# Kernel tuning notes

Hardware: AMD Instinct MI355X
Metric: run time of the kernel (lower is better)

The kernel has to match this reference:

```python
import jax, jax.numpy as jnp
import numpy as np

B, F, N = 128, 256, 2000

def setup_inputs() -> dict:
    key = jax.random.key(0)
    ks = jax.random.split(key, 10)
    s = 0.05
    return {
        'nfeature': jax.random.normal(ks[0], (B, F, N, 1), jnp.float32),
        'last_current': jax.random.randint(ks[1], (B, 2), 0, N, jnp.int32),
        'Wg': jax.random.normal(ks[2], (F, F), jnp.float32) * s,
        'bg': jax.random.normal(ks[3], (F,), jnp.float32) * s,
        'Wnode': jax.random.normal(ks[4], (3 * F, F), jnp.float32) * s,
        'bnode': jax.random.normal(ks[5], (3 * F,), jnp.float32) * s,
        'Wlc': jax.random.normal(ks[6], (F, 2 * F), jnp.float32) * s,
        'blc': jax.random.normal(ks[7], (F,), jnp.float32) * s,
        'Wproj': jax.random.normal(ks[8], (F, F), jnp.float32) * s,
        'bproj': jax.random.normal(ks[9], (F,), jnp.float32) * s,
    }

def reference(nfeature, last_current, Wg, bg, Wnode, bnode, Wlc, blc, Wproj, bproj):
    # nfeature: [B, F, N, 1]
    x = nfeature[..., 0]                                  # [B, F, N]
    f = x.shape[1]
    scale = 1.0 / jnp.sqrt(jnp.asarray(f, x.dtype))
    # global fixed query: max over nodes then Linear
    glb = jnp.max(x, axis=2)                              # [B, F]
    Q = glb @ Wg.T + bg                                   # [B, F]
    # node embeddings via 1x1 conv == channel GEMM, split into K, V, logit_K
    kvl = jnp.einsum('bfn,gf->bgn', x, Wnode) + bnode[None, :, None]  # [B, 3F, N]
    K, V, Klog = jnp.split(kvl, 3, axis=1)                # each [B, F, N]
    # gather last/current city features
    lc = jnp.take_along_axis(x, last_current[:, None, :], axis=2)     # [B, F, 2]
    context = jnp.concatenate([lc[:, :, 0], lc[:, :, 1]], axis=1)     # [B, 2F]
    cQ = context @ Wlc.T + blc + Q                        # [B, F]
    # attention: single query over N keys
    ucj = jnp.einsum('bf,bfn->bn', cQ, K) * scale         # [B, N]
    attn = jax.nn.softmax(ucj, axis=1)
    nc = jnp.einsum('bn,bfn->bf', attn, V)                # [B, F]
    nc = nc @ Wproj.T + bproj                             # [B, F]
    logits = jnp.einsum('bf,bfn->bn', nc, Klog) * scale   # [B, N]
    return jnp.tanh(logits) * 10.0
```

## Files before the change

kernel.cpp:

```cpp
#include <hip/hip_runtime.h>
#include <hip/hip_fp16.h>
#include <math.h>

#define BB 128
#define FF 256
#define NN 2000
#define SW 8
#define SC 256

typedef float f32x4 __attribute__((ext_vector_type(4)));
union H8 { f32x4 v; __half2 h[4]; };

__device__ __forceinline__ float sel8(f32x4 a, f32x4 b, int e) {
    float v;
    switch (e) {
        case 0: v = a.x; break; case 1: v = a.y; break;
        case 2: v = a.z; break; case 3: v = a.w; break;
        case 4: v = b.x; break; case 5: v = b.y; break;
        case 6: v = b.z; break; default: v = b.w; break;
    }
    return v;
}

__device__ __forceinline__ float dot4(f32x4 a, f32x4 b) {
    float s = a.x * b.x;
    s = fmaf(a.y, b.y, s);
    s = fmaf(a.z, b.z, s);
    s = fmaf(a.w, b.w, s);
    return s;
}

__global__ __launch_bounds__(256) void k_convmax(const float* __restrict__ x,
                                                 const int* __restrict__ lc,
                                                 __half* __restrict__ xh,
                                                 float* __restrict__ glb,
                                                 float* __restrict__ xg) {
    int row  = (blockIdx.x << 2) | (threadIdx.x >> 6);
    int lane = threadIdx.x & 63;
    int b    = row >> 8;
    const int c0 = lc[2 * b], c1 = lc[2 * b + 1];
    const int i0 = c0 >> 3, e0 = c0 & 7;
    const int i1 = c1 >> 3, e1 = c1 & 7;
    const f32x4* src = (const f32x4*)(x + (size_t)row * NN);
    f32x4*       dst = (f32x4*)(xh + (size_t)row * NN);
    float m = -INFINITY;
    for (int i = lane; i < 250; i += 64) {
        f32x4 a = __builtin_nontemporal_load(src + 2 * i);
        f32x4 q = __builtin_nontemporal_load(src + 2 * i + 1);
        m = fmaxf(m, fmaxf(fmaxf(a.x, a.y), fmaxf(a.z, a.w)));
        m = fmaxf(m, fmaxf(fmaxf(q.x, q.y), fmaxf(q.z, q.w)));
        if (i == i0) xg[row * 2]     = sel8(a, q, e0);
        if (i == i1) xg[row * 2 + 1] = sel8(a, q, e1);
        H8 o;
        o.h[0] = __floats2half2_rn(a.x, a.y);
        o.h[1] = __floats2half2_rn(a.z, a.w);
        o.h[2] = __floats2half2_rn(q.x, q.y);
        o.h[3] = __floats2half2_rn(q.z, q.w);
        dst[i] = o.v;
    }
#pragma unroll
    for (int off = 32; off; off >>= 1) m = fmaxf(m, __shfl_xor(m, off));
    if (!lane) glb[row] = m;
}

__global__ __launch_bounds__(256) void k_prep(
    const float* __restrict__ xg, const float* __restrict__ glb,
    const float* __restrict__ Wg, const float* __restrict__ bg,
    const float* __restrict__ Wnode, const float* __restrict__ bnode,
    const float* __restrict__ Wlc, const float* __restrict__ blc,
    float* __restrict__ cK, float* __restrict__ cK0)
{
    int b = blockIdx.x, tid = threadIdx.x, w = tid >> 6, lane = tid & 63;
    __shared__ float s_glb[FF], s_ctx[2 * FF], s_cQ[FF], s_bias[FF], s_red[FF];
    s_glb[tid] = glb[b * FF + tid];
    float2 g2 = ((const float2*)xg)[b * FF + tid];
    s_ctx[tid]      = g2.x;
    s_ctx[FF + tid] = g2.y;
    s_bias[tid] = bg[tid] + blc[tid];
    __syncthreads();

    f32x4 gv  = *(const f32x4*)&s_glb[lane << 2];
    f32x4 c0v = *(const f32x4*)&s_ctx[lane << 3];
    f32x4 c1v = *(const f32x4*)&s_ctx[(lane << 3) + 4];

    for (int k = 0; k < 64; k += 4) {
        float p0, p1, p2, p3;
        {
            int fb = (w << 6) + k;
            f32x4 wg0 = *(const f32x4*)(Wg + (size_t)fb * FF + (lane << 2));
            f32x4 wg1 = *(const f32x4*)(Wg + (size_t)(fb + 1) * FF + (lane << 2));
            f32x4 wg2 = *(const f32x4*)(Wg + (size_t)(fb + 2) * FF + (lane << 2));
            f32x4 wg3 = *(const f32x4*)(Wg + (size_t)(fb + 3) * FF + (lane << 2));
            f32x4 wa0 = *(const f32x4*)(Wlc + (size_t)fb * 2 * FF + (lane << 3));
            f32x4 wb0 = *(const f32x4*)(Wlc + (size_t)fb * 2 * FF + (lane << 3) + 4);
            f32x4 wa1 = *(const f32x4*)(Wlc + (size_t)(fb + 1) * 2 * FF + (lane << 3));
            f32x4 wb1 = *(const f32x4*)(Wlc + (size_t)(fb + 1) * 2 * FF + (lane << 3) + 4);
            f32x4 wa2 = *(const f32x4*)(Wlc + (size_t)(fb + 2) * 2 * FF + (lane << 3));
            f32x4 wb2 = *(const f32x4*)(Wlc + (size_t)(fb + 2) * 2 * FF + (lane << 3) + 4);
            f32x4 wa3 = *(const f32x4*)(Wlc + (size_t)(fb + 3) * 2 * FF + (lane << 3));
            f32x4 wb3 = *(const f32x4*)(Wlc + (size_t)(fb + 3) * 2 * FF + (lane << 3) + 4);
            p0 = dot4(wg0, gv) + dot4(wa0, c0v) + dot4(wb0, c1v);
            p1 = dot4(wg1, gv) + dot4(wa1, c0v) + dot4(wb1, c1v);
            p2 = dot4(wg2, gv) + dot4(wa2, c0v) + dot4(wb2, c1v);
            p3 = dot4(wg3, gv) + dot4(wa3, c0v) + dot4(wb3, c1v);
        }
#pragma unroll
        for (int off = 32; off; off >>= 1) {
            p0 += __shfl_xor(p0, off);
            p1 += __shfl_xor(p1, off);
            p2 += __shfl_xor(p2, off);
            p3 += __shfl_xor(p3, off);
        }
        if (lane == 0) {
            int fb = (w << 6) + k;
            s_cQ[fb]     = p0 + s_bias[fb];
            s_cQ[fb + 1] = p1 + s_bias[fb + 1];
            s_cQ[fb + 2] = p2 + s_bias[fb + 2];
            s_cQ[fb + 3] = p3 + s_bias[fb + 3];
        }
    }
    __syncthreads();

    {
        float a0 = 0, a1 = 0, a2 = 0, a3 = 0, a4 = 0, a5 = 0, a6 = 0, a7 = 0;
        for (int g = 0; g < FF; g += 8) {
            float w0 = Wnode[(size_t)(g + 0) * FF + tid];
            float w1 = Wnode[(size_t)(g + 1) * FF + tid];
            float w2 = Wnode[(size_t)(g + 2) * FF + tid];
            float w3 = Wnode[(size_t)(g + 3) * FF + tid];
            float w4 = Wnode[(size_t)(g + 4) * FF + tid];
            float w5 = Wnode[(size_t)(g + 5) * FF + tid];
            float w6 = Wnode[(size_t)(g + 6) * FF + tid];
            float w7 = Wnode[(size_t)(g + 7) * FF + tid];
            a0 = fmaf(s_cQ[g + 0], w0, a0); a1 = fmaf(s_cQ[g + 1], w1, a1);
            a2 = fmaf(s_cQ[g + 2], w2, a2); a3 = fmaf(s_cQ[g + 3], w3, a3);
            a4 = fmaf(s_cQ[g + 4], w4, a4); a5 = fmaf(s_cQ[g + 5], w5, a5);
            a6 = fmaf(s_cQ[g + 6], w6, a6); a7 = fmaf(s_cQ[g + 7], w7, a7);
        }
        cK[b * FF + tid] = ((a0 + a1) + (a2 + a3)) + ((a4 + a5) + (a6 + a7));
    }
    s_red[tid] = s_cQ[tid] * bnode[tid];
    __syncthreads();
    for (int s = 128; s > 0; s >>= 1) {
        if (tid < s) s_red[tid] += s_red[tid + s];
        __syncthreads();
    }
    if (tid == 0) cK0[b] = s_red[0];
}

__global__ __launch_bounds__(512) void k_attn(
    const __half* __restrict__ xh,
    const float* __restrict__ cK, const float* __restrict__ cK0,
    float* __restrict__ y_part, float* __restrict__ m_part,
    float* __restrict__ s_part)
{
    int b = blockIdx.x >> 3, st = blockIdx.x & 7;
    int tid = threadIdx.x, w = tid >> 6, lane = tid & 63;
    int par = lane >> 5, chunk = lane & 31;
    __shared__ __half tile[FF][SC];
    __shared__ float s_u[8][SC];
    __shared__ float s_p[SC];
    __shared__ float s_cK[FF];
    __shared__ float s_red[8], s_red2[8];
    if (tid < FF) s_cK[tid] = cK[b * FF + tid];
    __syncthreads();

    int colbase = (st << 8) + (chunk << 3);
    bool cvalid = colbase < NN;
    const __half* base = xh + ((size_t)(b * FF) + (w << 5) + par) * NN + colbase;

    float up0 = 0, up1 = 0, up2 = 0, up3 = 0, up4 = 0, up5 = 0, up6 = 0, up7 = 0;
#pragma unroll
    for (int g = 0; g < 4; ++g) {
        f32x4 hv[4];
#pragma unroll
        for (int r = 0; r < 4; ++r) {
            if (cvalid) hv[r] = *(const f32x4*)(base + (size_t)((g << 3) + (r << 1)) * NN);
            else        hv[r] = (f32x4){0.f, 0.f, 0.f, 0.f};
        }
#pragma unroll
        for (int r = 0; r < 4; ++r) {
            int row = (w << 5) + par + (g << 3) + (r << 1);
            *(f32x4*)&tile[row][(chunk ^ (row & 7)) << 3] = hv[r];
            H8 u; u.v = hv[r];
            float c = s_cK[row];
            float2 q0 = __half22float2(u.h[0]);
            float2 q1 = __half22float2(u.h[1]);
            float2 q2 = __half22float2(u.h[2]);
            float2 q3 = __half22float2(u.h[3]);
            up0 = fmaf(c, q0.x, up0); up1 = fmaf(c, q0.y, up1);
            up2 = fmaf(c, q1.x, up2); up3 = fmaf(c, q1.y, up3);
            up4 = fmaf(c, q2.x, up4); up5 = fmaf(c, q2.y, up5);
            up6 = fmaf(c, q3.x, up6); up7 = fmaf(c, q3.y, up7);
        }
    }
    up0 += __shfl_xor(up0, 32); up1 += __shfl_xor(up1, 32);
    up2 += __shfl_xor(up2, 32); up3 += __shfl_xor(up3, 32);
    up4 += __shfl_xor(up4, 32); up5 += __shfl_xor(up5, 32);
    up6 += __shfl_xor(up6, 32); up7 += __shfl_xor(up7, 32);
    if (!par) {
        f32x4 v0 = {up0, up1, up2, up3}, v1 = {up4, up5, up6, up7};
        *(f32x4*)&s_u[w][chunk << 3]       = v0;
        *(f32x4*)&s_u[w][(chunk << 3) + 4] = v1;
    }
    __syncthreads();

    const float scale = 0.0625f;
    float uu = -INFINITY;
    if (tid < SC) {
        int col = (st << 8) + tid;
        if (col < NN) {
            float usum = 0.f;
#pragma unroll
            for (int ww = 0; ww < 8; ++ww) usum += s_u[ww][tid];
            uu = (usum + cK0[b]) * scale;
        }
    }
    float m = uu;
#pragma unroll
    for (int off = 32; off; off >>= 1) m = fmaxf(m, __shfl_xor(m, off));
    if (!lane && w < 4) s_red[w] = m;
    __syncthreads();
    float M = fmaxf(fmaxf(s_red[0], s_red[1]), fmaxf(s_red[2], s_red[3]));
    float e = (uu > -INFINITY) ? __expf(uu - M) : 0.f;
    if (tid < SC) s_p[tid] = e;
    float ssum = e;
#pragma unroll
    for (int off = 32; off; off >>= 1) ssum += __shfl_xor(ssum, off);
    if (!lane && w < 4) s_red2[w] = ssum;
    __syncthreads();
    if (!tid) {
        m_part[(b << 3) + st] = M;
        s_part[(b << 3) + st] = s_red2[0] + s_red2[1] + s_red2[2] + s_red2[3];
    }

    f32x4 pv0 = *(const f32x4*)&s_p[chunk << 3];
    f32x4 pv1 = *(const f32x4*)&s_p[(chunk << 3) + 4];
    float acc[16];
#pragma unroll
    for (int k = 0; k < 16; ++k) {
        int row = (w << 5) + par + (k << 1);
        H8 u; u.v = *(const f32x4*)&tile[row][(chunk ^ (row & 7)) << 3];
        float2 q0 = __half22float2(u.h[0]);
        float2 q1 = __half22float2(u.h[1]);
        float2 q2 = __half22float2(u.h[2]);
        float2 q3 = __half22float2(u.h[3]);
        float a = 0.f;
        a = fmaf(pv0.x, q0.x, a); a = fmaf(pv0.y, q0.y, a);
        a = fmaf(pv0.z, q1.x, a); a = fmaf(pv0.w, q1.y, a);
        a = fmaf(pv1.x, q2.x, a); a = fmaf(pv1.y, q2.y, a);
        a = fmaf(pv1.z, q3.x, a); a = fmaf(pv1.w, q3.y, a);
        acc[k] = a;
    }
    __syncthreads();
    float* tbuf = (float*)&tile[0][0];
#pragma unroll
    for (int k = 0; k < 16; ++k)
        tbuf[(w << 10) + ((par + (k << 1)) << 5) + chunk] = acc[k];
    __syncthreads();
    {
        int row = tid >> 1, half = tid & 1;
        const float* srcp = tbuf + ((row >> 5) << 10) + ((row & 31) << 5) + (half << 4);
        f32x4 a0 = *(const f32x4*)srcp;
        f32x4 a1 = *(const f32x4*)(srcp + 4);
        f32x4 a2 = *(const f32x4*)(srcp + 8);
        f32x4 a3 = *(const f32x4*)(srcp + 12);
        float sm = ((a0.x + a0.y) + (a0.z + a0.w)) + ((a1.x + a1.y) + (a1.z + a1.w)) +
                   ((a2.x + a2.y) + (a2.z + a2.w)) + ((a3.x + a3.y) + (a3.z + a3.w));
        sm += __shfl_xor(sm, 1);
        if (!half) y_part[(size_t)((b << 3) + st) * FF + row] = sm;
    }
}

__global__ __launch_bounds__(256) void k_dense(
    const float* __restrict__ y_part, const float* __restrict__ m_part,
    const float* __restrict__ s_part,
    const float* __restrict__ Wnode, const float* __restrict__ bnode,
    const float* __restrict__ Wproj, const float* __restrict__ bproj,
    float* __restrict__ cL, float* __restrict__ cL0)
{
    int b = blockIdx.x, tid = threadIdx.x, w = tid >> 6, lane = tid & 63;
    __shared__ float s_y[FF], s_v[FF], s_n[FF], s_b1[FF], s_b2[FF], s_red[FF];

    s_b1[tid] = bnode[FF + tid];
    s_b2[tid] = bproj[tid];
    float M = -INFINITY;
#pragma unroll
    for (int s = 0; s < 8; ++s) M = fmaxf(M, m_part[(b << 3) + s]);
    float S = 0.f, wgt[8];
#pragma unroll
    for (int s = 0; s < 8; ++s) {
        wgt[s] = __expf(m_part[(b << 3) + s] - M);
        S = fmaf(wgt[s], s_part[(b << 3) + s], S);
    }
    float invS = 1.0f / S;
    float acc = 0.f;
#pragma unroll
    for (int s = 0; s < 8; ++s)
        acc = fmaf(wgt[s], y_part[(size_t)((b << 3) + s) * FF + tid], acc);
    s_y[tid] = acc * invS;
    __syncthreads();

    {
        f32x4 yv = *(const f32x4*)&s_y[lane << 2];
        for (int k = 0; k < 64; k += 4) {
            int fb = (w << 6) + k;
            f32x4 w0 = *(const f32x4*)(Wnode + (size_t)(FF + fb) * FF + (lane << 2));
            f32x4 w1 = *(const f32x4*)(Wnode + (size_t)(FF + fb + 1) * FF + (lane << 2));
            f32x4 w2 = *(const f32x4*)(Wnode + (size_t)(FF + fb + 2) * FF + (lane << 2));
            f32x4 w3 = *(const f32x4*)(Wnode + (size_t)(FF + fb + 3) * FF + (lane << 2));
            float p0 = dot4(w0, yv), p1 = dot4(w1, yv), p2 = dot4(w2, yv), p3 = dot4(w3, yv);
#pragma unroll
            for (int off = 32; off; off >>= 1) {
                p0 += __shfl_xor(p0, off);
                p1 += __shfl_xor(p1, off);
                p2 += __shfl_xor(p2, off);
                p3 += __shfl_xor(p3, off);
            }
            if (lane == 0) {
                s_v[fb]     = p0 + s_b1[fb];
                s_v[fb + 1] = p1 + s_b1[fb + 1];
                s_v[fb + 2] = p2 + s_b1[fb + 2];
                s_v[fb + 3] = p3 + s_b1[fb + 3];
            }
        }
    }
    __syncthreads();
    {
        f32x4 vv = *(const f32x4*)&s_v[lane << 2];
        for (int k = 0; k < 64; k += 4) {
            int fb = (w << 6) + k;
            f32x4 w0 = *(const f32x4*)(Wproj + (size_t)fb * FF + (lane << 2));
            f32x4 w1 = *(const f32x4*)(Wproj + (size_t)(fb + 1) * FF + (lane << 2));
            f32x4 w2 = *(const f32x4*)(Wproj + (size_t)(fb + 2) * FF + (lane << 2));
            f32x4 w3 = *(const f32x4*)(Wproj + (size_t)(fb + 3) * FF + (lane << 2));
            float p0 = dot4(w0, vv), p1 = dot4(w1, vv), p2 = dot4(w2, vv), p3 = dot4(w3, vv);
#pragma unroll
            for (int off = 32; off; off >>= 1) {
                p0 += __shfl_xor(p0, off);
                p1 += __shfl_xor(p1, off);
                p2 += __shfl_xor(p2, off);
                p3 += __shfl_xor(p3, off);
            }
            if (lane == 0) {
                s_n[fb]     = p0 + s_b2[fb];
                s_n[fb + 1] = p1 + s_b2[fb + 1];
                s_n[fb + 2] = p2 + s_b2[fb + 2];
                s_n[fb + 3] = p3 + s_b2[fb + 3];
            }
        }
    }
    __syncthreads();
    {
        float a0 = 0, a1 = 0, a2 = 0, a3 = 0, a4 = 0, a5 = 0, a6 = 0, a7 = 0;
        for (int g = 0; g < FF; g += 8) {
            float w0 = Wnode[(size_t)(2 * FF + g + 0) * FF + tid];
            float w1 = Wnode[(size_t)(2 * FF + g + 1) * FF + tid];
            float w2 = Wnode[(size_t)(2 * FF + g + 2) * FF + tid];
            float w3 = Wnode[(size_t)(2 * FF + g + 3) * FF + tid];
            float w4 = Wnode[(size_t)(2 * FF + g + 4) * FF + tid];
            float w5 = Wnode[(size_t)(2 * FF + g + 5) * FF + tid];
            float w6 = Wnode[(size_t)(2 * FF + g + 6) * FF + tid];
            float w7 = Wnode[(size_t)(2 * FF + g + 7) * FF + tid];
            a0 = fmaf(s_n[g + 0], w0, a0); a1 = fmaf(s_n[g + 1], w1, a1);
            a2 = fmaf(s_n[g + 2], w2, a2); a3 = fmaf(s_n[g + 3], w3, a3);
            a4 = fmaf(s_n[g + 4], w4, a4); a5 = fmaf(s_n[g + 5], w5, a5);
            a6 = fmaf(s_n[g + 6], w6, a6); a7 = fmaf(s_n[g + 7], w7, a7);
        }
        cL[b * FF + tid] = ((a0 + a1) + (a2 + a3)) + ((a4 + a5) + (a6 + a7));
    }
    s_red[tid] = s_n[tid] * bnode[2 * FF + tid];
    __syncthreads();
    for (int s = 128; s > 0; s >>= 1) {
        if (tid < s) s_red[tid] += s_red[tid + s];
        __syncthreads();
    }
    if (tid == 0) cL0[b] = s_red[0];
}

__global__ __launch_bounds__(512) void k_logits(const __half* __restrict__ xh,
                                                const float* __restrict__ cL,
                                                const float* __restrict__ cL0,
                                                float* __restrict__ out)
{
    int b = blockIdx.x >> 3, st = blockIdx.x & 7;
    int tid = threadIdx.x, w = tid >> 6, lane = tid & 63;
    int par = lane >> 5, chunk = lane & 31;
    __shared__ float s_cL[FF];
    __shared__ float s_acc[8][SC];
    if (tid < FF) s_cL[tid] = cL[b * FF + tid];
    __syncthreads();

    int colbase = (st << 8) + (chunk << 3);
    bool cvalid = colbase < NN;
    const __half* base = xh + ((size_t)(b * FF) + (w << 5) + par) * NN + colbase;
    float up0 = 0, up1 = 0, up2 = 0, up3 = 0, up4 = 0, up5 = 0, up6 = 0, up7 = 0;
    if (cvalid) {
#pragma unroll
        for (int g = 0; g < 4; ++g) {
            f32x4 hv[4];
#pragma unroll
            for (int r = 0; r < 4; ++r)
                hv[r] = *(const f32x4*)(base + (size_t)((g << 3) + (r << 1)) * NN);
#pragma unroll
            for (int r = 0; r < 4; ++r) {
                int row = (w << 5) + par + (g << 3) + (r << 1);
                H8 u; u.v = hv[r];
                float c = s_cL[row];
                float2 q0 = __half22float2(u.h[0]);
                float2 q1 = __half22float2(u.h[1]);
                float2 q2 = __half22float2(u.h[2]);
                float2 q3 = __half22float2(u.h[3]);
                up0 = fmaf(c, q0.x, up0); up1 = fmaf(c, q0.y, up1);
                up2 = fmaf(c, q1.x, up2); up3 = fmaf(c, q1.y, up3);
                up4 = fmaf(c, q2.x, up4); up5 = fmaf(c, q2.y, up5);
                up6 = fmaf(c, q3.x, up6); up7 = fmaf(c, q3.y, up7);
            }
        }
    }
    up0 += __shfl_xor(up0, 32); up1 += __shfl_xor(up1, 32);
    up2 += __shfl_xor(up2, 32); up3 += __shfl_xor(up3, 32);
    up4 += __shfl_xor(up4, 32); up5 += __shfl_xor(up5, 32);
    up6 += __shfl_xor(up6, 32); up7 += __shfl_xor(up7, 32);
    if (!par) {
        f32x4 v0 = {up0, up1, up2, up3}, v1 = {up4, up5, up6, up7};
        *(f32x4*)&s_acc[w][chunk << 3]       = v0;
        *(f32x4*)&s_acc[w][(chunk << 3) + 4] = v1;
    }
    __syncthreads();
    if (tid < SC) {
        int col = (st << 8) + tid;
        if (col < NN) {
            float t = 0.f;
#pragma unroll
            for (int ww = 0; ww < 8; ++ww) t += s_acc[ww][tid];
            out[(size_t)b * NN + col] = tanhf((t + cL0[b]) * 0.0625f) * 10.f;
        }
    }
}

extern "C" void kernel_launch(void* const* d_in, const int* in_sizes, int n_in,
                              void* d_out, int out_size, void* d_ws, size_t ws_size,
                              hipStream_t stream) {
    const float* x     = (const float*)d_in[0];
    const int*   lc    = (const int*)d_in[1];
    const float* Wg    = (const float*)d_in[2];
    const float* bg    = (const float*)d_in[3];
    const float* Wnode = (const float*)d_in[4];
    const float* bnode = (const float*)d_in[5];
    const float* Wlc   = (const float*)d_in[6];
    const float* blc   = (const float*)d_in[7];
    const float* Wproj = (const float*)d_in[8];
    const float* bproj = (const float*)d_in[9];
    float* out = (float*)d_out;

    float* ws     = (float*)d_ws;
    float* glb    = ws + 0;
    float* xg     = ws + 32768;
    float* cK     = ws + 98304;
    float* cK0    = ws + 131072;
    float* m_part = ws + 132096;
    float* s_part = ws + 134144;
    float* cL     = ws + 136192;
    float* cL0    = ws + 168960;
    float* y_part = ws + 169984;
    __half* xh    = (__half*)(ws + (2 << 20));

    k_convmax<<<BB * FF / 4, 256, 0, stream>>>(x, lc, xh, glb, xg);
    k_prep   <<<BB, 256, 0, stream>>>(xg, glb, Wg, bg, Wnode, bnode, Wlc, blc, cK, cK0);
    k_attn   <<<BB * SW, 512, 0, stream>>>(xh, cK, cK0, y_part, m_part, s_part);
    k_dense  <<<BB, 256, 0, stream>>>(y_part, m_part, s_part, Wnode, bnode, Wproj, bproj, cL, cL0);
    k_logits <<<BB * SW, 512, 0, stream>>>(xh, cL, cL0, out);
}
```

Measured before the change: 182.8 us.

## Split attention into 16 column slices and keep the x tile in registers

k_attn now processes 128-column slices, so there are 16 blocks per batch instead of 8. Each thread keeps its eight fp16 row vectors in registers and reuses them for both the score pass and the weighted-V pass. This drops the 128KB shared-memory tile and one block-wide barrier, which should allow more blocks per CU and remove the LDS round trip. k_dense now merges 16 partial softmax results, and k_logits batches its loads in groups of eight. The trade-off is higher register pressure, more partial results to merge, and reliance on wavefront-local ordering when reading tbuf.

```diff
diff --git a/kernel.cpp b/kernel.cpp
--- a/kernel.cpp
+++ b/kernel.cpp
@@ -5,8 +5,10 @@
 #define BB 128
 #define FF 256
 #define NN 2000
-#define SW 8
-#define SC 256
+#define SWA 16
+#define SCA 128
+#define SWL 8
+#define SCL 256
 
 typedef float f32x4 __attribute__((ext_vector_type(4)));
 union H8 { f32x4 v; __half2 h[4]; };
@@ -154,52 +156,52 @@
     float* __restrict__ y_part, float* __restrict__ m_part,
     float* __restrict__ s_part)
 {
-    int b = blockIdx.x >> 3, st = blockIdx.x & 7;
+    int b = blockIdx.x >> 4, st = blockIdx.x & 15;
     int tid = threadIdx.x, w = tid >> 6, lane = tid & 63;
-    int par = lane >> 5, chunk = lane & 31;
-    __shared__ __half tile[FF][SC];
-    __shared__ float s_u[8][SC];
-    __shared__ float s_p[SC];
+    int par = lane >> 4, chunk = lane & 15;
+    __shared__ float tbuf[8][512];
+    __shared__ float s_u[8][SCA];
+    __shared__ float s_p[SCA];
     __shared__ float s_cK[FF];
     __shared__ float s_red[8], s_red2[8];
     if (tid < FF) s_cK[tid] = cK[b * FF + tid];
     __syncthreads();
 
-    int colbase = (st << 8) + (chunk << 3);
+    int colbase = (st << 7) + (chunk << 3);
     bool cvalid = colbase < NN;
     const __half* base = xh + ((size_t)(b * FF) + (w << 5) + par) * NN + colbase;
-
-    float up0 = 0, up1 = 0, up2 = 0, up3 = 0, up4 = 0, up5 = 0, up6 = 0, up7 = 0;
-#pragma unroll
-    for (int g = 0; g < 4; ++g) {
-        f32x4 hv[4];
-#pragma unroll
-        for (int r = 0; r < 4; ++r) {
-            if (cvalid) hv[r] = *(const f32x4*)(base + (size_t)((g << 3) + (r << 1)) * NN);
-            else        hv[r] = (f32x4){0.f, 0.f, 0.f, 0.f};
-        }
-#pragma unroll
-        for (int r = 0; r < 4; ++r) {
-            int row = (w << 5) + par + (g << 3) + (r << 1);
-            *(f32x4*)&tile[row][(chunk ^ (row & 7)) << 3] = hv[r];
-            H8 u; u.v = hv[r];
-            float c = s_cK[row];
-            float2 q0 = __half22float2(u.h[0]);
-            float2 q1 = __half22float2(u.h[1]);
-            float2 q2 = __half22float2(u.h[2]);
-            float2 q3 = __half22float2(u.h[3]);
-            up0 = fmaf(c, q0.x, up0); up1 = fmaf(c, q0.y, up1);
-            up2 = fmaf(c, q1.x, up2); up3 = fmaf(c, q1.y, up3);
-            up4 = fmaf(c, q2.x, up4); up5 = fmaf(c, q2.y, up5);
-            up6 = fmaf(c, q3.x, up6); up7 = fmaf(c, q3.y, up7);
-        }
-    }
-    up0 += __shfl_xor(up0, 32); up1 += __shfl_xor(up1, 32);
-    up2 += __shfl_xor(up2, 32); up3 += __shfl_xor(up3, 32);
-    up4 += __shfl_xor(up4, 32); up5 += __shfl_xor(up5, 32);
-    up6 += __shfl_xor(up6, 32); up7 += __shfl_xor(up7, 32);
-    if (!par) {
-        f32x4 v0 = {up0, up1, up2, up3}, v1 = {up4, up5, up6, up7};
+    const f32x4 zero = {0.f, 0.f, 0.f, 0.f};
+
+    f32x4 hv[8];
+#pragma unroll
+    for (int r = 0; r < 8; ++r)
+        hv[r] = cvalid ? *(const f32x4*)(base + (size_t)(r << 2) * NN) : zero;
+
+    float uc0 = 0, uc1 = 0, uc2 = 0, uc3 = 0, uc4 = 0, uc5 = 0, uc6 = 0, uc7 = 0;
+#pragma unroll
+    for (int r = 0; r < 8; ++r) {
+        int row = (w << 5) + (r << 2) + par;
+        H8 u; u.v = hv[r];
+        float c = s_cK[row];
+        float2 q0 = __half22float2(u.h[0]);
+        float2 q1 = __half22float2(u.h[1]);
+        float2 q2 = __half22float2(u.h[2]);
+        float2 q3 = __half22float2(u.h[3]);
+        uc0 = fmaf(c, q0.x, uc0); uc1 = fmaf(c, q0.y, uc1);
+        uc2 = fmaf(c, q1.x, uc2); uc3 = fmaf(c, q1.y, uc3);
+        uc4 = fmaf(c, q2.x, uc4); uc5 = fmaf(c, q2.y, uc5);
+        uc6 = fmaf(c, q3.x, uc6); uc7 = fmaf(c, q3.y, uc7);
+    }
+    uc0 += __shfl_xor(uc0, 16); uc0 += __shfl_xor(uc0, 32);
+    uc1 += __shfl_xor(uc1, 16); uc1 += __shfl_xor(uc1, 32);
+    uc2 += __shfl_xor(uc2, 16); uc2 += __shfl_xor(uc2, 32);
+    uc3 += __shfl_xor(uc3, 16); uc3 += __shfl_xor(uc3, 32);
+    uc4 += __shfl_xor(uc4, 16); uc4 += __shfl_xor(uc4, 32);
+    uc5 += __shfl_xor(uc5, 16); uc5 += __shfl_xor(uc5, 32);
+    uc6 += __shfl_xor(uc6, 16); uc6 += __shfl_xor(uc6, 32);
+    uc7 += __shfl_xor(uc7, 16); uc7 += __shfl_xor(uc7, 32);
+    if (par == 0) {
+        f32x4 v0 = {uc0, uc1, uc2, uc3}, v1 = {uc4, uc5, uc6, uc7};
         *(f32x4*)&s_u[w][chunk << 3]       = v0;
         *(f32x4*)&s_u[w][(chunk << 3) + 4] = v1;
     }
@@ -207,8 +209,8 @@
 
     const float scale = 0.0625f;
     float uu = -INFINITY;
-    if (tid < SC) {
-        int col = (st << 8) + tid;
+    if (tid < SCA) {
+        int col = (st << 7) + tid;
         if (col < NN) {
             float usum = 0.f;
 #pragma unroll
@@ -219,28 +221,26 @@
     float m = uu;
 #pragma unroll
     for (int off = 32; off; off >>= 1) m = fmaxf(m, __shfl_xor(m, off));
-    if (!lane && w < 4) s_red[w] = m;
-    __syncthreads();
-    float M = fmaxf(fmaxf(s_red[0], s_red[1]), fmaxf(s_red[2], s_red[3]));
+    if (!lane && w < 2) s_red[w] = m;
+    __syncthreads();
+    float M = fmaxf(s_red[0], s_red[1]);
     float e = (uu > -INFINITY) ? __expf(uu - M) : 0.f;
-    if (tid < SC) s_p[tid] = e;
+    if (tid < SCA) s_p[tid] = e;
     float ssum = e;
 #pragma unroll
     for (int off = 32; off; off >>= 1) ssum += __shfl_xor(ssum, off);
-    if (!lane && w < 4) s_red2[w] = ssum;
+    if (!lane && w < 2) s_red2[w] = ssum;
     __syncthreads();
     if (!tid) {
-        m_part[(b << 3) + st] = M;
-        s_part[(b << 3) + st] = s_red2[0] + s_red2[1] + s_red2[2] + s_red2[3];
+        m_part[(b << 4) + st] = M;
+        s_part[(b << 4) + st] = s_red2[0] + s_red2[1];
     }
 
     f32x4 pv0 = *(const f32x4*)&s_p[chunk << 3];
     f32x4 pv1 = *(const f32x4*)&s_p[(chunk << 3) + 4];
-    float acc[16];
-#pragma unroll
-    for (int k = 0; k < 16; ++k) {
-        int row = (w << 5) + par + (k << 1);
-        H8 u; u.v = *(const f32x4*)&tile[row][(chunk ^ (row & 7)) << 3];
+#pragma unroll
+    for (int r = 0; r < 8; ++r) {
+        H8 u; u.v = hv[r];
         float2 q0 = __half22float2(u.h[0]);
         float2 q1 = __half22float2(u.h[1]);
         float2 q2 = __half22float2(u.h[2]);
@@ -250,25 +250,16 @@
         a = fmaf(pv0.z, q1.x, a); a = fmaf(pv0.w, q1.y, a);
         a = fmaf(pv1.x, q2.x, a); a = fmaf(pv1.y, q2.y, a);
         a = fmaf(pv1.z, q3.x, a); a = fmaf(pv1.w, q3.y, a);
-        acc[k] = a;
-    }
-    __syncthreads();
-    float* tbuf = (float*)&tile[0][0];
-#pragma unroll
-    for (int k = 0; k < 16; ++k)
-        tbuf[(w << 10) + ((par + (k << 1)) << 5) + chunk] = acc[k];
-    __syncthreads();
+        tbuf[w][(((r << 2) + par) << 4) + chunk] = a;
+    }
     {
         int row = tid >> 1, half = tid & 1;
-        const float* srcp = tbuf + ((row >> 5) << 10) + ((row & 31) << 5) + (half << 4);
+        const float* srcp = &tbuf[row >> 5][((row & 31) << 4) + (half << 3)];
         f32x4 a0 = *(const f32x4*)srcp;
         f32x4 a1 = *(const f32x4*)(srcp + 4);
-        f32x4 a2 = *(const f32x4*)(srcp + 8);
-        f32x4 a3 = *(const f32x4*)(srcp + 12);
-        float sm = ((a0.x + a0.y) + (a0.z + a0.w)) + ((a1.x + a1.y) + (a1.z + a1.w)) +
-                   ((a2.x + a2.y) + (a2.z + a2.w)) + ((a3.x + a3.y) + (a3.z + a3.w));
+        float sm = ((a0.x + a0.y) + (a0.z + a0.w)) + ((a1.x + a1.y) + (a1.z + a1.w));
         sm += __shfl_xor(sm, 1);
-        if (!half) y_part[(size_t)((b << 3) + st) * FF + row] = sm;
+        if (!half) y_part[(size_t)((b << 4) + st) * FF + row] = sm;
     }
 }
 
@@ -286,18 +277,18 @@
     s_b2[tid] = bproj[tid];
     float M = -INFINITY;
 #pragma unroll
-    for (int s = 0; s < 8; ++s) M = fmaxf(M, m_part[(b << 3) + s]);
-    float S = 0.f, wgt[8];
-#pragma unroll
-    for (int s = 0; s < 8; ++s) {
-        wgt[s] = __expf(m_part[(b << 3) + s] - M);
-        S = fmaf(wgt[s], s_part[(b << 3) + s], S);
+    for (int s = 0; s < 16; ++s) M = fmaxf(M, m_part[(b << 4) + s]);
+    float S = 0.f, wgt[16];
+#pragma unroll
+    for (int s = 0; s < 16; ++s) {
+        wgt[s] = __expf(m_part[(b << 4) + s] - M);
+        S = fmaf(wgt[s], s_part[(b << 4) + s], S);
     }
     float invS = 1.0f / S;
     float acc = 0.f;
 #pragma unroll
-    for (int s = 0; s < 8; ++s)
-        acc = fmaf(wgt[s], y_part[(size_t)((b << 3) + s) * FF + tid], acc);
+    for (int s = 0; s < 16; ++s)
+        acc = fmaf(wgt[s], y_part[(size_t)((b << 4) + s) * FF + tid], acc);
     s_y[tid] = acc * invS;
     __syncthreads();
 
@@ -387,35 +378,34 @@
     int tid = threadIdx.x, w = tid >> 6, lane = tid & 63;
     int par = lane >> 5, chunk = lane & 31;
     __shared__ float s_cL[FF];
-    __shared__ float s_acc[8][SC];
+    __shared__ float s_acc[8][SCL];
     if (tid < FF) s_cL[tid] = cL[b * FF + tid];
     __syncthreads();
 
     int colbase = (st << 8) + (chunk << 3);
     bool cvalid = colbase < NN;
     const __half* base = xh + ((size_t)(b * FF) + (w << 5) + par) * NN + colbase;
+    const f32x4 zero = {0.f, 0.f, 0.f, 0.f};
     float up0 = 0, up1 = 0, up2 = 0, up3 = 0, up4 = 0, up5 = 0, up6 = 0, up7 = 0;
-    if (cvalid) {
-#pragma unroll
-        for (int g = 0; g < 4; ++g) {
-            f32x4 hv[4];
-#pragma unroll
-            for (int r = 0; r < 4; ++r)
-                hv[r] = *(const f32x4*)(base + (size_t)((g << 3) + (r << 1)) * NN);
-#pragma unroll
-            for (int r = 0; r < 4; ++r) {
-                int row = (w << 5) + par + (g << 3) + (r << 1);
-                H8 u; u.v = hv[r];
-                float c = s_cL[row];
-                float2 q0 = __half22float2(u.h[0]);
-                float2 q1 = __half22float2(u.h[1]);
-                float2 q2 = __half22float2(u.h[2]);
-                float2 q3 = __half22float2(u.h[3]);
-                up0 = fmaf(c, q0.x, up0); up1 = fmaf(c, q0.y, up1);
-                up2 = fmaf(c, q1.x, up2); up3 = fmaf(c, q1.y, up3);
-                up4 = fmaf(c, q2.x, up4); up5 = fmaf(c, q2.y, up5);
-                up6 = fmaf(c, q3.x, up6); up7 = fmaf(c, q3.y, up7);
-            }
+#pragma unroll
+    for (int h = 0; h < 2; ++h) {
+        f32x4 hv[8];
+#pragma unroll
+        for (int r = 0; r < 8; ++r)
+            hv[r] = cvalid ? *(const f32x4*)(base + (size_t)((h << 4) + (r << 1)) * NN) : zero;
+#pragma unroll
+        for (int r = 0; r < 8; ++r) {
+            int row = (w << 5) + par + (h << 4) + (r << 1);
+            H8 u; u.v = hv[r];
+            float c = s_cL[row];
+            float2 q0 = __half22float2(u.h[0]);
+            float2 q1 = __half22float2(u.h[1]);
+            float2 q2 = __half22float2(u.h[2]);
+            float2 q3 = __half22float2(u.h[3]);
+            up0 = fmaf(c, q0.x, up0); up1 = fmaf(c, q0.y, up1);
+            up2 = fmaf(c, q1.x, up2); up3 = fmaf(c, q1.y, up3);
+            up4 = fmaf(c, q2.x, up4); up5 = fmaf(c, q2.y, up5);
+            up6 = fmaf(c, q3.x, up6); up7 = fmaf(c, q3.y, up7);
         }
     }
     up0 += __shfl_xor(up0, 32); up1 += __shfl_xor(up1, 32);
@@ -428,7 +418,7 @@
         *(f32x4*)&s_acc[w][(chunk << 3) + 4] = v1;
     }
     __syncthreads();
-    if (tid < SC) {
+    if (tid < SCL) {
         int col = (st << 8) + tid;
         if (col < NN) {
             float t = 0.f;
@@ -468,7 +458,7 @@
 
     k_convmax<<<BB * FF / 4, 256, 0, stream>>>(x, lc, xh, glb, xg);
     k_prep   <<<BB, 256, 0, stream>>>(xg, glb, Wg, bg, Wnode, bnode, Wlc, blc, cK, cK0);
-    k_attn   <<<BB * SW, 512, 0, stream>>>(xh, cK, cK0, y_part, m_part, s_part);
+    k_attn   <<<BB * SWA, 512, 0, stream>>>(xh, cK, cK0, y_part, m_part, s_part);
     k_dense  <<<BB, 256, 0, stream>>>(y_part, m_part, s_part, Wnode, bnode, Wproj, bproj, cL, cL0);
-    k_logits <<<BB * SW, 512, 0, stream>>>(xh, cL, cL0, out);
-}
+    k_logits <<<BB * SWL, 512, 0, stream>>>(xh, cL, cL0, out);
+}
```

After: 177.5 us. -2.9%, faster.
